# Performance work log

Measured on AMD Instinct MI355X. Metric: run time of the kernel, lower is better.

The kernel has to match this reference:

```python
import jax, jax.numpy as jnp
import numpy as np

X_SIZE = 256
H_SIZE = 512
N_CHILDREN = 32768


def setup_inputs() -> dict:
    key = jax.random.key(0)
    ks = jax.random.split(key, 7)
    x = jax.random.normal(ks[0], (X_SIZE,), dtype=jnp.float32)
    hs = jax.random.normal(ks[1], (N_CHILDREN, H_SIZE), dtype=jnp.float32)
    cs = jax.random.normal(ks[2], (N_CHILDREN, H_SIZE), dtype=jnp.float32)
    # xavier-uniform-ish init for weights, zeros for biases
    def xavier(k, shape):
        fan_in, fan_out = shape[-1], shape[-2]
        limit = float(np.sqrt(6.0 / (fan_in + fan_out)))
        return jax.random.uniform(k, shape, jnp.float32, -limit, limit)
    w_iou = xavier(ks[3], (3, H_SIZE, X_SIZE))
    u_iou = xavier(ks[4], (3, H_SIZE, H_SIZE))
    b_iou = jnp.zeros((3, H_SIZE), jnp.float32)
    w_f = xavier(ks[5], (H_SIZE, X_SIZE))
    u_f = xavier(ks[6], (H_SIZE, H_SIZE))
    b_f = jnp.zeros((H_SIZE, 1), jnp.float32)
    return {"x": x, "hs": hs, "cs": cs, "w_iou": w_iou, "u_iou": u_iou,
            "b_iou": b_iou, "w_f": w_f, "u_f": u_f, "b_f": b_f}


def reference(x, hs, cs, w_iou, u_iou, b_iou, w_f, u_f, b_f):
    # Child-sum Tree-LSTM cell for a single node.
    h_sum = hs.sum(axis=0)                                    # (h,)
    iou = (jnp.einsum('khx,x->kh', w_iou, x)
           + jnp.einsum('khg,g->kh', u_iou, h_sum)
           + b_iou)                                            # (3, h)
    i, o, u = iou[0], iou[1], iou[2]
    # fs: (h, n_children) forget gates, one per child
    fs = (w_f @ x)[:, None] + jnp.einsum('hg,ng->hn', u_f, hs) + b_f
    i = jax.nn.sigmoid(i)
    o = jax.nn.sigmoid(o)
    fs = jax.nn.sigmoid(fs)
    u = jnp.tanh(u)
    c = i * u + jnp.sum(fs * cs.T, axis=1)                    # (h,)
    h = o * jnp.tanh(c)
    return (h, c)
```

## Files before the change

kernel.cpp:

```cpp
#include <hip/hip_runtime.h>
#include <stdint.h>
#include <stddef.h>

#define H 512
#define XD 256
#define NCHLD 32768
#define BM 128
#define BN 128
#define KTP 64
#define NPH 8
#define BP 68
#define NSHARD 32

#define WS_PREF 0
#define WS_IOU  512
#define WS_CACC 2048
#define WS_HSUM 18432
#define WS_UF16 34816

typedef float f32x4 __attribute__((ext_vector_type(4)));
typedef _Float16 f16x8 __attribute__((ext_vector_type(8)));
typedef _Float16 f16x4 __attribute__((ext_vector_type(4)));

__device__ __forceinline__ float sigm(float x) { return 1.0f / (1.0f + __expf(-x)); }

__device__ __forceinline__ void gload_lds16(const _Float16* g, void* l) {
    __builtin_amdgcn_global_load_lds((const __attribute__((address_space(1))) void*)g,
                                     (__attribute__((address_space(3))) void*)l,
                                     16, 0, 0);
}

__global__ __launch_bounds__(256) void k0_setup(const float* __restrict__ x,
                                                const float* __restrict__ w_f,
                                                const float* __restrict__ b_f,
                                                const float* __restrict__ u_f,
                                                float* __restrict__ ws) {
    const int b = blockIdx.x;
    if (b < 256) {
        const int i = (b * 256 + threadIdx.x) * 4;
        float4 v = *(const float4*)(u_f + i);
        f16x4 h;
        h[0] = (_Float16)v.x; h[1] = (_Float16)v.y;
        h[2] = (_Float16)v.z; h[3] = (_Float16)v.w;
        *(f16x4*)((_Float16*)(ws + WS_UF16) + i) = h;
    } else {
        const int gid = (b - 256) * 256 + threadIdx.x;
        const int row = gid >> 2;
        const int part = gid & 3;
        const float4* wr = (const float4*)(w_f + (size_t)row * XD) + part * 16;
        const float4* xv = (const float4*)x + part * 16;
        float acc = 0.0f;
#pragma unroll 4
        for (int i = 0; i < 16; ++i) {
            float4 a = wr[i], c = xv[i];
            acc += a.x * c.x + a.y * c.y + a.z * c.z + a.w * c.w;
        }
        acc += __shfl_xor(acc, 1);
        acc += __shfl_xor(acc, 2);
        if (part == 0) ws[WS_PREF + row] = acc + b_f[row];
        float4 z = make_float4(0.f, 0.f, 0.f, 0.f);
#pragma unroll
        for (int t = 0; t < 4; ++t)
            ((float4*)ws)[512 + gid * 4 + t] = z;
    }
}

__global__ __launch_bounds__(512, 4) void k2_main(const float* __restrict__ hs,
                                                  const float* __restrict__ cs,
                                                  float* __restrict__ ws) {
    __shared__ _Float16 As[2][BM * 64];
    __shared__ _Float16 Bs[2][BN][BP];
    __shared__ float hsum_l[H];

    const _Float16* uf16 = (const _Float16*)(ws + WS_UF16);
    const float* pre_f = ws + WS_PREF;
    const int bid   = blockIdx.x;
    const int ntile = bid >> 2;
    const int mtile = bid & 3;
    const int c0    = ntile * BN;
    const int r0    = mtile * BM;

    const int tid  = threadIdx.x;
    const int wid  = tid >> 6;
    const int lane = tid & 63;

    const int ch = tid >> 2;
    const int kq = tid & 3;
    const float4* bsrc = (const float4*)(hs + (size_t)(c0 + ch) * H) + kq * 4;

    const int dd0  = wid * 128 + lane;
    const int row0 = dd0 >> 3;
    const int sl0  = (dd0 & 7) ^ (row0 & 7);
    const _Float16* asrc0 = uf16 + (size_t)(r0 + row0) * H + sl0 * 8;
    const int dd1  = dd0 + 64;
    const int row1 = dd1 >> 3;
    const int sl1  = (dd1 & 7) ^ (row1 & 7);
    const _Float16* asrc1 = uf16 + (size_t)(r0 + row1) * H + sl1 * 8;

    const int wm = wid >> 1;
    const int wn = wid & 1;
    const int fc = lane & 15;
    const int q  = lane >> 4;

#define ISSUE_A(p, buf)                                                          \
    {                                                                            \
        gload_lds16(asrc0 + (p) * KTP, (char*)&As[buf][0] + (wid * 128) * 16);   \
        gload_lds16(asrc1 + (p) * KTP, (char*)&As[buf][0] + (wid * 128 + 64) * 16); \
    }

#define WRITE_B(p, buf, b0, b1, b2, b3)                                          \
    {                                                                            \
        _Float16* bd = &Bs[buf][ch][kq * 16];                                    \
        f16x8 lo, hi;                                                            \
        lo[0] = (_Float16)(b0).x; lo[1] = (_Float16)(b0).y;                      \
        lo[2] = (_Float16)(b0).z; lo[3] = (_Float16)(b0).w;                      \
        lo[4] = (_Float16)(b1).x; lo[5] = (_Float16)(b1).y;                      \
        lo[6] = (_Float16)(b1).z; lo[7] = (_Float16)(b1).w;                      \
        hi[0] = (_Float16)(b2).x; hi[1] = (_Float16)(b2).y;                      \
        hi[2] = (_Float16)(b2).z; hi[3] = (_Float16)(b2).w;                      \
        hi[4] = (_Float16)(b3).x; hi[5] = (_Float16)(b3).y;                      \
        hi[6] = (_Float16)(b3).z; hi[7] = (_Float16)(b3).w;                      \
        *(f16x8*)bd = lo;                                                        \
        *(f16x8*)(bd + 8) = hi;                                                  \
        if (mtile == 0) {                                                        \
            float4 v0 = b0, v1 = b1, v2 = b2, v3 = b3;                           \
            _Pragma("unroll")                                                    \
            for (int m = 4; m <= 32; m <<= 1) {                                  \
                v0.x += __shfl_xor(v0.x, m); v0.y += __shfl_xor(v0.y, m);        \
                v0.z += __shfl_xor(v0.z, m); v0.w += __shfl_xor(v0.w, m);        \
                v1.x += __shfl_xor(v1.x, m); v1.y += __shfl_xor(v1.y, m);        \
                v1.z += __shfl_xor(v1.z, m); v1.w += __shfl_xor(v1.w, m);        \
                v2.x += __shfl_xor(v2.x, m); v2.y += __shfl_xor(v2.y, m);        \
                v2.z += __shfl_xor(v2.z, m); v2.w += __shfl_xor(v2.w, m);        \
                v3.x += __shfl_xor(v3.x, m); v3.y += __shfl_xor(v3.y, m);        \
                v3.z += __shfl_xor(v3.z, m); v3.w += __shfl_xor(v3.w, m);        \
            }                                                                    \
            if (lane < 4) {                                                      \
                float* hd = &hsum_l[(p) * KTP + lane * 16];                      \
                atomicAdd(hd + 0,  v0.x); atomicAdd(hd + 1,  v0.y);              \
                atomicAdd(hd + 2,  v0.z); atomicAdd(hd + 3,  v0.w);              \
                atomicAdd(hd + 4,  v1.x); atomicAdd(hd + 5,  v1.y);              \
                atomicAdd(hd + 6,  v1.z); atomicAdd(hd + 7,  v1.w);              \
                atomicAdd(hd + 8,  v2.x); atomicAdd(hd + 9,  v2.y);              \
                atomicAdd(hd + 10, v2.z); atomicAdd(hd + 11, v2.w);              \
                atomicAdd(hd + 12, v3.x); atomicAdd(hd + 13, v3.y);              \
                atomicAdd(hd + 14, v3.z); atomicAdd(hd + 15, v3.w);              \
            }                                                                    \
        }                                                                        \
    }

    ISSUE_A(0, 0)
    float4 b0 = bsrc[0], b1 = bsrc[1], b2 = bsrc[2], b3 = bsrc[3];
    if (tid < H) hsum_l[tid] = 0.0f;
    __syncthreads();
    WRITE_B(0, 0, b0, b1, b2, b3)
    __syncthreads();

    f32x4 acc[2][4];
    const f32x4 vzero = {0.0f, 0.0f, 0.0f, 0.0f};
#pragma unroll
    for (int rt = 0; rt < 2; ++rt)
#pragma unroll
        for (int ct = 0; ct < 4; ++ct)
            acc[rt][ct] = vzero;

    int cur = 0;
#pragma unroll
    for (int p = 0; p < NPH; ++p) {
        float4 n0, n1, n2, n3;
        if (p + 1 < NPH) {
            ISSUE_A(p + 1, cur ^ 1)
            const float4* bs = bsrc + (p + 1) * 16;
            n0 = bs[0]; n1 = bs[1]; n2 = bs[2]; n3 = bs[3];
        }

#pragma unroll
        for (int kk = 0; kk < 2; ++kk) {
            f16x8 af[2];
#pragma unroll
            for (int rt = 0; rt < 2; ++rt) {
                const int ar  = wm * 32 + rt * 16 + fc;
                const int seg = (kk * 4 + q) ^ (ar & 7);
                af[rt] = *(const f16x8*)((const char*)&As[cur][0] + ar * 128 + seg * 16);
            }
#pragma unroll
            for (int ct = 0; ct < 4; ++ct) {
                const f16x8 bf = *(const f16x8*)(&Bs[cur][wn * 64 + ct * 16 + fc][kk * 32 + q * 8]);
                acc[0][ct] = __builtin_amdgcn_mfma_f32_16x16x32_f16(af[0], bf, acc[0][ct], 0, 0, 0);
                acc[1][ct] = __builtin_amdgcn_mfma_f32_16x16x32_f16(af[1], bf, acc[1][ct], 0, 0, 0);
            }
        }

        if (p + 1 < NPH) {
            WRITE_B(p + 1, cur ^ 1, n0, n1, n2, n3)
            __syncthreads();
            cur ^= 1;
        }
    }
#undef ISSUE_A
#undef WRITE_B

    if (mtile == 0)
        atomicAdd(&ws[WS_HSUM + (ntile & (NSHARD - 1)) * H + tid], hsum_l[tid]);

    float* c_acc = ws + WS_CACC + (bid & (NSHARD - 1)) * H;
#pragma unroll
    for (int rt = 0; rt < 2; ++rt) {
        const int rglob = r0 + wm * 32 + rt * 16 + q * 4;
        float4 pf = *(const float4*)(pre_f + rglob);
        f32x4 csum = vzero;
#pragma unroll
        for (int ct = 0; ct < 4; ++ct) {
            const int child = c0 + wn * 64 + ct * 16 + fc;
            float4 cv = *(const float4*)(cs + (size_t)child * H + rglob);
            csum[0] += sigm(acc[rt][ct][0] + pf.x) * cv.x;
            csum[1] += sigm(acc[rt][ct][1] + pf.y) * cv.y;
            csum[2] += sigm(acc[rt][ct][2] + pf.z) * cv.z;
            csum[3] += sigm(acc[rt][ct][3] + pf.w) * cv.w;
        }
#pragma unroll
        for (int m = 1; m <= 8; m <<= 1) {
            csum[0] += __shfl_xor(csum[0], m); csum[1] += __shfl_xor(csum[1], m);
            csum[2] += __shfl_xor(csum[2], m); csum[3] += __shfl_xor(csum[3], m);
        }
        if (fc == 0) {
            atomicAdd(&c_acc[rglob + 0], csum[0]); atomicAdd(&c_acc[rglob + 1], csum[1]);
            atomicAdd(&c_acc[rglob + 2], csum[2]); atomicAdd(&c_acc[rglob + 3], csum[3]);
        }
    }
}

__global__ __launch_bounds__(256) void k3_iou(const float* __restrict__ x,
                                              const float* __restrict__ w_iou,
                                              const float* __restrict__ u_iou,
                                              const float* __restrict__ b_iou,
                                              float* __restrict__ ws) {
    __shared__ float h_red[H];
    const int tid = threadIdx.x;
    {
        float a0 = 0.0f, a1 = 0.0f;
#pragma unroll 8
        for (int s = 0; s < NSHARD; ++s) {
            a0 += ws[WS_HSUM + s * H + tid * 2 + 0];
            a1 += ws[WS_HSUM + s * H + tid * 2 + 1];
        }
        h_red[tid * 2 + 0] = a0;
        h_red[tid * 2 + 1] = a1;
    }
    __syncthreads();

    const int gid = blockIdx.x * 256 + tid;
    const int row = gid >> 4;
    const int part = gid & 15;
    float acc = 0.0f;
    const float4* wr = (const float4*)(w_iou + (size_t)row * XD) + part * 4;
    const float4* xv = (const float4*)x + part * 4;
#pragma unroll
    for (int i = 0; i < 4; ++i) {
        float4 a = wr[i], b = xv[i];
        acc += a.x * b.x + a.y * b.y + a.z * b.z + a.w * b.w;
    }
    const float4* ur = (const float4*)(u_iou + (size_t)row * H) + part * 8;
    const float4* hv = (const float4*)h_red + part * 8;
#pragma unroll
    for (int i = 0; i < 8; ++i) {
        float4 a = ur[i], b = hv[i];
        acc += a.x * b.x + a.y * b.y + a.z * b.z + a.w * b.w;
    }
    acc += __shfl_xor(acc, 1);
    acc += __shfl_xor(acc, 2);
    acc += __shfl_xor(acc, 4);
    acc += __shfl_xor(acc, 8);
    if (part == 0) ws[WS_IOU + row] = acc + b_iou[row];
}

__global__ __launch_bounds__(512) void k4_fin(const float* __restrict__ ws,
                                              float* __restrict__ out) {
    const int h = threadIdx.x;
    float cacc = 0.0f;
#pragma unroll 8
    for (int s = 0; s < NSHARD; ++s) cacc += ws[WS_CACC + s * H + h];
    const float i = sigm(ws[WS_IOU + h]);
    const float o = sigm(ws[WS_IOU + 512 + h]);
    const float u = tanhf(ws[WS_IOU + 1024 + h]);
    const float c = i * u + cacc;
    out[h]       = o * tanhf(c);
    out[512 + h] = c;
}

extern "C" void kernel_launch(void* const* d_in, const int* in_sizes, int n_in,
                              void* d_out, int out_size, void* d_ws, size_t ws_size,
                              hipStream_t stream) {
    const float* x     = (const float*)d_in[0];
    const float* hs    = (const float*)d_in[1];
    const float* cs    = (const float*)d_in[2];
    const float* w_iou = (const float*)d_in[3];
    const float* u_iou = (const float*)d_in[4];
    const float* b_iou = (const float*)d_in[5];
    const float* w_f   = (const float*)d_in[6];
    const float* u_f   = (const float*)d_in[7];
    const float* b_f   = (const float*)d_in[8];
    float* ws  = (float*)d_ws;
    float* out = (float*)d_out;

    k0_setup<<<264, 256, 0, stream>>>(x, w_f, b_f, u_f, ws);
    k2_main<<<(NCHLD / BN) * (H / BM), 512, 0, stream>>>(hs, cs, ws);
    k3_iou<<<96, 256, 0, stream>>>(x, w_iou, u_iou, b_iou, ws);
    k4_fin<<<1, 512, 0, stream>>>(ws, out);
}
```

Measured before the change: 251.8 us.

## Restructure forget-gate GEMM to full-row tiles and split hsum into own kernel

The main GEMM kernel now assigns each block 64 children across all 512 hidden rows, loading the whole child tile of hs (converted to fp16, XOR-swizzled) into LDS once. The u_f operand is read directly from global/L2 instead of being double-buffered through LDS. The hs column sum moves to a separate k1_hsum kernel. This removes the 4x redundant hs reads across m-tiles and the per-phase barriers. In exchange hs is read one extra time for the sum, and every block streams the full u_f matrix from cache.

```diff
diff --git a/kernel.cpp b/kernel.cpp
--- a/kernel.cpp
+++ b/kernel.cpp
@@ -5,11 +5,7 @@
 #define H 512
 #define XD 256
 #define NCHLD 32768
-#define BM 128
-#define BN 128
-#define KTP 64
-#define NPH 8
-#define BP 68
+#define NB 64
 #define NSHARD 32
 
 #define WS_PREF 0
@@ -23,12 +19,6 @@
 typedef _Float16 f16x4 __attribute__((ext_vector_type(4)));
 
 __device__ __forceinline__ float sigm(float x) { return 1.0f / (1.0f + __expf(-x)); }
-
-__device__ __forceinline__ void gload_lds16(const _Float16* g, void* l) {
-    __builtin_amdgcn_global_load_lds((const __attribute__((address_space(1))) void*)g,
-                                     (__attribute__((address_space(3))) void*)l,
-                                     16, 0, 0);
-}
 
 __global__ __launch_bounds__(256) void k0_setup(const float* __restrict__ x,
                                                 const float* __restrict__ w_f,
@@ -65,153 +55,113 @@
     }
 }
 
+__global__ __launch_bounds__(256) void k1_hsum(const float* __restrict__ hs,
+                                               float* __restrict__ ws) {
+    __shared__ float red[2][H];
+    const int t = threadIdx.x;
+    const int b = blockIdx.x;
+    const float4* src = (const float4*)hs + (size_t)b * 64 * 128 + (t >> 7) * 128 + (t & 127);
+    float4 a = make_float4(0.f, 0.f, 0.f, 0.f);
+#pragma unroll
+    for (int i = 0; i < 32; ++i) {
+        float4 v = src[(size_t)i * 256];
+        a.x += v.x; a.y += v.y; a.z += v.z; a.w += v.w;
+    }
+    *(float4*)&red[t >> 7][(t & 127) * 4] = a;
+    __syncthreads();
+    float* shard = ws + WS_HSUM + (b & (NSHARD - 1)) * H;
+    atomicAdd(&shard[t],       red[0][t]       + red[1][t]);
+    atomicAdd(&shard[t + 256], red[0][t + 256] + red[1][t + 256]);
+}
+
 __global__ __launch_bounds__(512, 4) void k2_main(const float* __restrict__ hs,
                                                   const float* __restrict__ cs,
                                                   float* __restrict__ ws) {
-    __shared__ _Float16 As[2][BM * 64];
-    __shared__ _Float16 Bs[2][BN][BP];
-    __shared__ float hsum_l[H];
+    __shared__ _Float16 Bs[NB * H];
 
     const _Float16* uf16 = (const _Float16*)(ws + WS_UF16);
     const float* pre_f = ws + WS_PREF;
-    const int bid   = blockIdx.x;
-    const int ntile = bid >> 2;
-    const int mtile = bid & 3;
-    const int c0    = ntile * BN;
-    const int r0    = mtile * BM;
+    float* c_acc = ws + WS_CACC + (blockIdx.x & (NSHARD - 1)) * H;
 
     const int tid  = threadIdx.x;
     const int wid  = tid >> 6;
     const int lane = tid & 63;
-
-    const int ch = tid >> 2;
-    const int kq = tid & 3;
-    const float4* bsrc = (const float4*)(hs + (size_t)(c0 + ch) * H) + kq * 4;
-
-    const int dd0  = wid * 128 + lane;
-    const int row0 = dd0 >> 3;
-    const int sl0  = (dd0 & 7) ^ (row0 & 7);
-    const _Float16* asrc0 = uf16 + (size_t)(r0 + row0) * H + sl0 * 8;
-    const int dd1  = dd0 + 64;
-    const int row1 = dd1 >> 3;
-    const int sl1  = (dd1 & 7) ^ (row1 & 7);
-    const _Float16* asrc1 = uf16 + (size_t)(r0 + row1) * H + sl1 * 8;
-
-    const int wm = wid >> 1;
-    const int wn = wid & 1;
-    const int fc = lane & 15;
-    const int q  = lane >> 4;
-
-#define ISSUE_A(p, buf)                                                          \
-    {                                                                            \
-        gload_lds16(asrc0 + (p) * KTP, (char*)&As[buf][0] + (wid * 128) * 16);   \
-        gload_lds16(asrc1 + (p) * KTP, (char*)&As[buf][0] + (wid * 128 + 64) * 16); \
-    }
-
-#define WRITE_B(p, buf, b0, b1, b2, b3)                                          \
-    {                                                                            \
-        _Float16* bd = &Bs[buf][ch][kq * 16];                                    \
-        f16x8 lo, hi;                                                            \
-        lo[0] = (_Float16)(b0).x; lo[1] = (_Float16)(b0).y;                      \
-        lo[2] = (_Float16)(b0).z; lo[3] = (_Float16)(b0).w;                      \
-        lo[4] = (_Float16)(b1).x; lo[5] = (_Float16)(b1).y;                      \
-        lo[6] = (_Float16)(b1).z; lo[7] = (_Float16)(b1).w;                      \
-        hi[0] = (_Float16)(b2).x; hi[1] = (_Float16)(b2).y;                      \
-        hi[2] = (_Float16)(b2).z; hi[3] = (_Float16)(b2).w;                      \
-        hi[4] = (_Float16)(b3).x; hi[5] = (_Float16)(b3).y;                      \
-        hi[6] = (_Float16)(b3).z; hi[7] = (_Float16)(b3).w;                      \
-        *(f16x8*)bd = lo;                                                        \
-        *(f16x8*)(bd + 8) = hi;                                                  \
-        if (mtile == 0) {                                                        \
-            float4 v0 = b0, v1 = b1, v2 = b2, v3 = b3;                           \
-            _Pragma("unroll")                                                    \
-            for (int m = 4; m <= 32; m <<= 1) {                                  \
-                v0.x += __shfl_xor(v0.x, m); v0.y += __shfl_xor(v0.y, m);        \
-                v0.z += __shfl_xor(v0.z, m); v0.w += __shfl_xor(v0.w, m);        \
-                v1.x += __shfl_xor(v1.x, m); v1.y += __shfl_xor(v1.y, m);        \
-                v1.z += __shfl_xor(v1.z, m); v1.w += __shfl_xor(v1.w, m);        \
-                v2.x += __shfl_xor(v2.x, m); v2.y += __shfl_xor(v2.y, m);        \
-                v2.z += __shfl_xor(v2.z, m); v2.w += __shfl_xor(v2.w, m);        \
-                v3.x += __shfl_xor(v3.x, m); v3.y += __shfl_xor(v3.y, m);        \
-                v3.z += __shfl_xor(v3.z, m); v3.w += __shfl_xor(v3.w, m);        \
-            }                                                                    \
-            if (lane < 4) {                                                      \
-                float* hd = &hsum_l[(p) * KTP + lane * 16];                      \
-                atomicAdd(hd + 0,  v0.x); atomicAdd(hd + 1,  v0.y);              \
-                atomicAdd(hd + 2,  v0.z); atomicAdd(hd + 3,  v0.w);              \
-                atomicAdd(hd + 4,  v1.x); atomicAdd(hd + 5,  v1.y);              \
-                atomicAdd(hd + 6,  v1.z); atomicAdd(hd + 7,  v1.w);              \
-                atomicAdd(hd + 8,  v2.x); atomicAdd(hd + 9,  v2.y);              \
-                atomicAdd(hd + 10, v2.z); atomicAdd(hd + 11, v2.w);              \
-                atomicAdd(hd + 12, v3.x); atomicAdd(hd + 13, v3.y);              \
-                atomicAdd(hd + 14, v3.z); atomicAdd(hd + 15, v3.w);              \
-            }                                                                    \
-        }                                                                        \
-    }
-
-    ISSUE_A(0, 0)
-    float4 b0 = bsrc[0], b1 = bsrc[1], b2 = bsrc[2], b3 = bsrc[3];
-    if (tid < H) hsum_l[tid] = 0.0f;
+    const int c0   = blockIdx.x * NB;
+    const int fc   = lane & 15;
+    const int q    = lane >> 4;
+
+    {
+        const float4* g0 = (const float4*)hs + (((size_t)(c0 + wid)) << 7) + (lane << 1);
+        _Float16* w0 = Bs + (wid << 9) + ((lane ^ wid) << 3);
+        float4 r0[8], r1[8];
+#pragma unroll
+        for (int j = 0; j < 4; ++j) {
+            r0[2 * j]     = g0[(size_t)j << 10];
+            r0[2 * j + 1] = g0[((size_t)j << 10) + 1];
+        }
+#pragma unroll
+        for (int j = 0; j < 4; ++j) {
+            r1[2 * j]     = g0[(size_t)(j + 4) << 10];
+            r1[2 * j + 1] = g0[((size_t)(j + 4) << 10) + 1];
+        }
+#pragma unroll
+        for (int j = 0; j < 4; ++j) {
+            f16x8 hv;
+            hv[0] = (_Float16)r0[2*j].x;   hv[1] = (_Float16)r0[2*j].y;
+            hv[2] = (_Float16)r0[2*j].z;   hv[3] = (_Float16)r0[2*j].w;
+            hv[4] = (_Float16)r0[2*j+1].x; hv[5] = (_Float16)r0[2*j+1].y;
+            hv[6] = (_Float16)r0[2*j+1].z; hv[7] = (_Float16)r0[2*j+1].w;
+            *(f16x8*)(w0 + (j << 12)) = hv;
+        }
+#pragma unroll
+        for (int j = 0; j < 4; ++j) {
+            f16x8 hv;
+            hv[0] = (_Float16)r1[2*j].x;   hv[1] = (_Float16)r1[2*j].y;
+            hv[2] = (_Float16)r1[2*j].z;   hv[3] = (_Float16)r1[2*j].w;
+            hv[4] = (_Float16)r1[2*j+1].x; hv[5] = (_Float16)r1[2*j+1].y;
+            hv[6] = (_Float16)r1[2*j+1].z; hv[7] = (_Float16)r1[2*j+1].w;
+            *(f16x8*)(w0 + ((j + 4) << 12)) = hv;
+        }
+    }
     __syncthreads();
-    WRITE_B(0, 0, b0, b1, b2, b3)
-    __syncthreads();
-
-    f32x4 acc[2][4];
+
+    f32x4 acc[4][4];
     const f32x4 vzero = {0.0f, 0.0f, 0.0f, 0.0f};
 #pragma unroll
-    for (int rt = 0; rt < 2; ++rt)
+    for (int rt = 0; rt < 4; ++rt)
 #pragma unroll
         for (int ct = 0; ct < 4; ++ct)
             acc[rt][ct] = vzero;
 
-    int cur = 0;
-#pragma unroll
-    for (int p = 0; p < NPH; ++p) {
-        float4 n0, n1, n2, n3;
-        if (p + 1 < NPH) {
-            ISSUE_A(p + 1, cur ^ 1)
-            const float4* bs = bsrc + (p + 1) * 16;
-            n0 = bs[0]; n1 = bs[1]; n2 = bs[2]; n3 = bs[3];
-        }
-
-#pragma unroll
-        for (int kk = 0; kk < 2; ++kk) {
-            f16x8 af[2];
-#pragma unroll
-            for (int rt = 0; rt < 2; ++rt) {
-                const int ar  = wm * 32 + rt * 16 + fc;
-                const int seg = (kk * 4 + q) ^ (ar & 7);
-                af[rt] = *(const f16x8*)((const char*)&As[cur][0] + ar * 128 + seg * 16);
-            }
-#pragma unroll
-            for (int ct = 0; ct < 4; ++ct) {
-                const f16x8 bf = *(const f16x8*)(&Bs[cur][wn * 64 + ct * 16 + fc][kk * 32 + q * 8]);
-                acc[0][ct] = __builtin_amdgcn_mfma_f32_16x16x32_f16(af[0], bf, acc[0][ct], 0, 0, 0);
-                acc[1][ct] = __builtin_amdgcn_mfma_f32_16x16x32_f16(af[1], bf, acc[1][ct], 0, 0, 0);
-            }
-        }
-
-        if (p + 1 < NPH) {
-            WRITE_B(p + 1, cur ^ 1, n0, n1, n2, n3)
-            __syncthreads();
-            cur ^= 1;
-        }
-    }
-#undef ISSUE_A
-#undef WRITE_B
-
-    if (mtile == 0)
-        atomicAdd(&ws[WS_HSUM + (ntile & (NSHARD - 1)) * H + tid], hsum_l[tid]);
-
-    float* c_acc = ws + WS_CACC + (bid & (NSHARD - 1)) * H;
-#pragma unroll
-    for (int rt = 0; rt < 2; ++rt) {
-        const int rglob = r0 + wm * 32 + rt * 16 + q * 4;
+    const _Float16* abase = uf16 + (size_t)(wid * 64 + fc) * H + q * 8;
+
+#pragma unroll
+    for (int kk = 0; kk < 16; ++kk) {
+        f16x8 af[4];
+#pragma unroll
+        for (int rt = 0; rt < 4; ++rt)
+            af[rt] = *(const f16x8*)(abase + (size_t)rt * 16 * H + kk * 32);
+        f16x8 bf[4];
+#pragma unroll
+        for (int ct = 0; ct < 4; ++ct) {
+            const int ch = ct * 16 + fc;
+            bf[ct] = *(const f16x8*)(Bs + ch * H + (((kk * 4 + q) ^ (fc & 7)) << 3));
+        }
+#pragma unroll
+        for (int ct = 0; ct < 4; ++ct)
+#pragma unroll
+            for (int rt = 0; rt < 4; ++rt)
+                acc[rt][ct] = __builtin_amdgcn_mfma_f32_16x16x32_f16(af[rt], bf[ct], acc[rt][ct], 0, 0, 0);
+    }
+
+#pragma unroll
+    for (int rt = 0; rt < 4; ++rt) {
+        const int rglob = wid * 64 + rt * 16 + q * 4;
         float4 pf = *(const float4*)(pre_f + rglob);
         f32x4 csum = vzero;
 #pragma unroll
         for (int ct = 0; ct < 4; ++ct) {
-            const int child = c0 + wn * 64 + ct * 16 + fc;
+            const int child = c0 + ct * 16 + fc;
             float4 cv = *(const float4*)(cs + (size_t)child * H + rglob);
             csum[0] += sigm(acc[rt][ct][0] + pf.x) * cv.x;
             csum[1] += sigm(acc[rt][ct][1] + pf.y) * cv.y;
@@ -304,7 +254,8 @@
     float* out = (float*)d_out;
 
     k0_setup<<<264, 256, 0, stream>>>(x, w_f, b_f, u_f, ws);
-    k2_main<<<(NCHLD / BN) * (H / BM), 512, 0, stream>>>(hs, cs, ws);
+    k1_hsum<<<512, 256, 0, stream>>>(hs, ws);
+    k2_main<<<NCHLD / NB, 512, 0, stream>>>(hs, cs, ws);
     k3_iou<<<96, 256, 0, stream>>>(x, w_iou, u_iou, b_iou, ws);
     k4_fin<<<1, 512, 0, stream>>>(ws, out);
 }
```

Result: faster. 220.9 us (-12.3%).
